# Performance work log

Measured on AMD Instinct MI355X. Metric: run time of the kernel, lower is better.

The kernel has to match this reference:

```python
import jax, jax.numpy as jnp
import numpy as np

F_DIM = 512   # feature_dim
H = 8         # num_heads
D = F_DIM // H  # attention_dim = 64
N = 12288     # total nodes
NP = 6144     # protein nodes (static)
NL = 3072     # ligand nodes (static)
EPS = 1e-5    # LayerNorm eps (torch default)


def setup_inputs() -> dict:
    key = jax.random.key(0)
    ks = jax.random.split(key, 12)
    g = lambda k, shape, s: (jax.random.normal(k, shape, jnp.float32) * s)
    return {
        "h": jax.random.normal(ks[0], (N, F_DIM), jnp.float32),
        # first NP active rows are protein (mask_ligand==0), next NL are ligand, rest inactive
        "mask_ligand": (jnp.arange(N) >= NP).astype(jnp.int32),
        "batch_mask": jnp.arange(N) < (NP + NL),
        "Wp": g(ks[1], (H, F_DIM, D), 0.04),   # per-head protein_linears (no bias)
        "Wl": g(ks[2], (H, F_DIM, D), 0.04),   # per-head ligand_linears (no bias)
        "Up_w": g(ks[3], (H, D, F_DIM), 0.1), "Up_b": g(ks[4], (H, F_DIM), 0.02),
        "Ul_w": g(ks[5], (H, D, F_DIM), 0.1), "Ul_b": g(ks[6], (H, F_DIM), 0.02),
        "ln_w": jnp.ones((D,), jnp.float32), "ln_b": jnp.zeros((D,), jnp.float32),
        "pg_w": g(ks[7], (F_DIM, D), 0.04), "pg_b": jnp.zeros((D,), jnp.float32),
        "lg_w": g(ks[8], (F_DIM, D), 0.04), "lg_b": jnp.zeros((D,), jnp.float32),
        "fb_w": g(ks[9], (D, D), 0.1), "fb_b": jnp.zeros((D,), jnp.float32),
        "fl_w": g(ks[10], (H * F_DIM, F_DIM), 0.015), "fl_b": g(ks[11], (F_DIM,), 0.02),
    }


def _layernorm(x, w, b):
    mu = x.mean(-1, keepdims=True)
    var = ((x - mu) ** 2).mean(-1, keepdims=True)
    return (x - mu) / jnp.sqrt(var + EPS) * w + b


def reference(h, mask_ligand, batch_mask, Wp, Wl, Up_w, Up_b, Ul_w, Ul_b,
              ln_w, ln_b, pg_w, pg_b, lg_w, lg_b, fb_w, fb_b, fl_w, fl_b):
    prot_idx = jnp.nonzero((mask_ligand == 0) & batch_mask, size=NP)[0]
    lig_idx = jnp.nonzero((mask_ligand == 1) & batch_mask, size=NL)[0]
    hp = h[prot_idx]   # [NP, F]
    hl = h[lig_idx]    # [NL, F]

    pf = jnp.einsum('nf,hfd->hnd', hp, Wp)              # per-head protein feats
    lf = jnp.einsum('mf,hfd->hmd', hl, Wl)              # per-head ligand feats
    scores = jnp.einsum('hnd,hmd->hnm', pf, lf) / (D ** 0.5)
    pa = jax.nn.softmax(scores, axis=-1)                # protein attends over ligand
    la = jax.nn.softmax(scores, axis=1)                 # ligand attends over protein
    pc = jnp.einsum('hnm,hmd->hnd', pa, lf)             # protein context
    lc = jnp.einsum('hnm,hnd->hmd', la, pf)             # ligand context

    # gates are head-independent in the original (recomputed identically per head)
    pgate = jax.nn.sigmoid(hp @ pg_w + pg_b)            # [NP, D]
    lgate = jax.nn.sigmoid(hl @ lg_w + lg_b)            # [NL, D]

    pc = jax.nn.sigmoid(_layernorm(pc * pgate, ln_w, ln_b) @ fb_w + fb_b)
    lc = jax.nn.sigmoid(_layernorm(lc * lgate, ln_w, ln_b) @ fb_w + fb_b)

    pout = jnp.einsum('hnd,hdf->hnf', pc, Up_w) + Up_b[:, None, :]
    lout = jnp.einsum('hmd,hdf->hmf', lc, Ul_w) + Ul_b[:, None, :]

    # concat per-head outputs along feature dim, then final projection
    p_final = pout.transpose(1, 0, 2).reshape(NP, H * F_DIM) @ fl_w + fl_b
    l_final = lout.transpose(1, 0, 2).reshape(NL, H * F_DIM) @ fl_w + fl_b

    h_updated = h.at[prot_idx].set(p_final + hp)
    h_updated = h_updated.at[lig_idx].set(l_final + hl)
    return h_updated
```

## Files before the change

kernel.cpp:

```cpp
#include <hip/hip_runtime.h>
#include <hip/hip_bf16.h>
#include <cstdint>
#include <cstddef>

#define F_DIM 512
#define NHEAD 8
#define DD 64
#define NPROT 6144
#define NLIG 3072
#define NACT 9216
#define NTOT 12288

typedef unsigned short u16;
typedef __attribute__((ext_vector_type(8))) short bf8;
typedef __attribute__((ext_vector_type(4))) float f4;

__device__ __forceinline__ u16 f2bf(float f){
  union { float f; uint32_t u; } v; v.f = f;
  uint32_t r = v.u + 0x7fffu + ((v.u >> 16) & 1u);
  return (u16)(r >> 16);
}

__device__ __forceinline__ f4 mfma16(bf8 a, bf8 b, f4 c){
  return __builtin_amdgcn_mfma_f32_16x16x32_bf16(a, b, c, 0, 0, 0);
}

__global__ void k_cvt(const float* __restrict__ in, u16* __restrict__ out, int n4){
  int i = blockIdx.x * blockDim.x + threadIdx.x;
  if (i >= n4) return;
  float4 v = ((const float4*)in)[i];
  union { u16 u[4]; uint64_t q; } pk;
  pk.u[0]=f2bf(v.x); pk.u[1]=f2bf(v.y); pk.u[2]=f2bf(v.z); pk.u[3]=f2bf(v.w);
  ((uint64_t*)out)[i] = pk.q;
}

__global__ __launch_bounds__(256) void k_cvtT64(const float* __restrict__ in,
                                                u16* __restrict__ out, int R, int C){
  __shared__ u16 T[64][65];
  int64_t base = (int64_t)blockIdx.z * R * C;
  int cb = blockIdx.x*64, rb = blockIdx.y*64;
  #pragma unroll
  for (int i=0;i<16;i++){
    int idx = i*256 + threadIdx.x;
    int r = idx>>6, c = idx&63;
    T[r][c] = f2bf(in[base + (int64_t)(rb+r)*C + cb + c]);
  }
  __syncthreads();
  #pragma unroll
  for (int i=0;i<16;i++){
    int idx = i*256 + threadIdx.x;
    int c = idx>>6, r = idx&63;
    out[base + (int64_t)(cb+c)*R + rb + r] = T[r][c];
  }
}

__global__ __launch_bounds__(256) void k_proj(const u16* __restrict__ hb,
    const u16* __restrict__ WpT, const u16* __restrict__ WlT,
    u16* __restrict__ pf, u16* __restrict__ pfT,
    u16* __restrict__ lfb, u16* __restrict__ lfT){
  int pass = blockIdx.z;
  if (pass == 1 && blockIdx.x >= NLIG/64) return;
  int M = pass ? NLIG : NPROT;
  const u16* A  = hb + (pass ? (size_t)NPROT*F_DIM : 0);
  const u16* BT = pass ? WlT : WpT;
  u16* P  = pass ? lfb : pf;
  u16* PT = pass ? lfT : pfT;
  int h = blockIdx.y;
  int w = threadIdx.x >> 6, lane = threadIdx.x & 63;
  int lr = lane & 15, lkg = lane >> 4, lk = lkg * 8;
  int rb = blockIdx.x * 64;
  const u16* Ap = A + (size_t)(rb + w*16 + lr) * F_DIM + lk;
  const u16* Bp = BT + (size_t)h * DD * F_DIM + (size_t)lr * F_DIM + lk;
  f4 acc[4] = {};
  for (int k = 0; k < F_DIM; k += 32){
    bf8 a = *(const bf8*)(Ap + k);
    #pragma unroll
    for (int cf = 0; cf < 4; cf++){
      bf8 b = *(const bf8*)(Bp + (size_t)cf*16*F_DIM + k);
      acc[cf] = mfma16(a, b, acc[cf]);
    }
  }
  __shared__ u16 T[64*72];
  #pragma unroll
  for (int cf = 0; cf < 4; cf++){
    int d = cf*16 + lr;
    #pragma unroll
    for (int r = 0; r < 4; r++){
      u16 v = f2bf(acc[cf][r]);
      int rl = w*16 + lkg*4 + r;
      P[(size_t)h*M*DD + (size_t)(rb+rl)*DD + d] = v;
      T[rl*72 + d] = v;
    }
  }
  __syncthreads();
  int d = threadIdx.x >> 2, j = threadIdx.x & 3;
  union { u16 u[16]; bf8 v[2]; } pk;
  #pragma unroll
  for (int uu = 0; uu < 16; uu++) pk.u[uu] = T[(j*16+uu)*72 + d];
  bf8* dst = (bf8*)(PT + ((size_t)h*DD + d)*M + rb + j*16);
  dst[0] = pk.v[0]; dst[1] = pk.v[1];
}

__global__ __launch_bounds__(256) void k_gate(const u16* __restrict__ hb,
    const u16* __restrict__ pgT, const u16* __restrict__ lgT,
    const float* __restrict__ pgb, const float* __restrict__ lgb,
    float* __restrict__ pgate, float* __restrict__ lgate){
  int pass = blockIdx.z;
  if (pass == 1 && blockIdx.x >= NLIG/64) return;
  const u16* A  = hb + (pass ? (size_t)NPROT*F_DIM : 0);
  const u16* BT = pass ? lgT : pgT;
  const float* gb = pass ? lgb : pgb;
  float* outp = pass ? lgate : pgate;
  int w = threadIdx.x>>6, lane = threadIdx.x&63, lr = lane&15, lkg = lane>>4, lk = lkg*8;
  int rb = blockIdx.x*64;
  const u16* Ap = A + (size_t)(rb + w*16 + lr)*F_DIM + lk;
  const u16* Bp = BT + (size_t)lr*F_DIM + lk;
  f4 acc[4] = {};
  for (int k=0;k<F_DIM;k+=32){
    bf8 a = *(const bf8*)(Ap+k);
    #pragma unroll
    for (int cf=0;cf<4;cf++){
      bf8 b = *(const bf8*)(Bp + (size_t)cf*16*F_DIM + k);
      acc[cf]=mfma16(a,b,acc[cf]);
    }
  }
  int r0 = rb + w*16 + lkg*4;
  #pragma unroll
  for (int cf=0;cf<4;cf++){
    int d = cf*16+lr; float bb = gb[d];
    #pragma unroll
    for (int r=0;r<4;r++){
      float z = acc[cf][r] + bb;
      outp[(size_t)(r0+r)*DD + d] = 1.f/(1.f + __expf(-z));
    }
  }
}

__global__ __launch_bounds__(256) void k_mw(const u16* __restrict__ UpWb, const u16* __restrict__ UlWb,
    const u16* __restrict__ flT, u16* __restrict__ MpT, u16* __restrict__ MlT){
  const u16* A = blockIdx.z ? UlWb : UpWb;
  u16* O = blockIdx.z ? MlT : MpT;
  int h = blockIdx.y;
  int fobase = blockIdx.x * 64;
  int w = threadIdx.x>>6, lane = threadIdx.x&63, lr = lane&15, lkg = lane>>4, lk = lkg*8;
  const u16* Ap = A + (size_t)h*DD*F_DIM + (size_t)(w*16+lr)*F_DIM + lk;
  const u16* Bp = flT + (size_t)(fobase+lr)*(NHEAD*F_DIM) + (size_t)h*F_DIM + lk;
  f4 acc[4] = {};
  for (int k=0;k<F_DIM;k+=32){
    bf8 a = *(const bf8*)(Ap+k);
    #pragma unroll
    for (int cf=0;cf<4;cf++){
      bf8 b = *(const bf8*)(Bp + (size_t)cf*16*(NHEAD*F_DIM) + k);
      acc[cf]=mfma16(a,b,acc[cf]);
    }
  }
  int d0 = w*16 + lkg*4;
  #pragma unroll
  for (int cf=0;cf<4;cf++){
    int fo = fobase + cf*16 + lr;
    #pragma unroll
    for (int r=0;r<4;r++)
      O[(size_t)fo*F_DIM + h*DD + d0 + r] = f2bf(acc[cf][r]);
  }
}

__global__ void k_cinit(const float* __restrict__ flb, float* __restrict__ cp, float* __restrict__ cl){
  int i = blockIdx.x*blockDim.x + threadIdx.x;
  if (i < F_DIM){ cp[i] = flb[i]; cl[i] = flb[i]; }
}
__global__ void k_cacc(const float* __restrict__ flw, const float* __restrict__ Upb,
    const float* __restrict__ Ulb, float* __restrict__ cp, float* __restrict__ cl){
  const float* bias = blockIdx.z ? Ulb : Upb;
  float* o = blockIdx.z ? cl : cp;
  int fo = blockIdx.y*256 + threadIdx.x;
  int r0 = blockIdx.x*512;
  float acc = 0.f;
  for (int r = r0; r < r0+512; r++) acc += bias[r] * flw[(size_t)r*F_DIM + fo];
  atomicAdd(o + fo, acc);
}

__global__ __launch_bounds__(256) void k_attn(
    const u16* __restrict__ pf, const u16* __restrict__ lfb,
    const u16* __restrict__ pfT, const u16* __restrict__ lfT,
    float* __restrict__ pnum, float* __restrict__ pden,
    float* __restrict__ lnum, float* __restrict__ lden){
  int bid = blockIdx.x;
  int pass = (bid >= 768);
  int NQ, NK, qt, chunk, h;
  const u16 *Q, *Kt, *Vt; float *num, *den;
  if (!pass){
    qt = bid >> 4; int rem = bid & 15; chunk = rem >> 3; h = rem & 7;
    NQ = NPROT; NK = NLIG; Q = pf; Kt = lfb; Vt = lfT; num = pnum; den = pden;
  } else {
    int l = bid - 768; qt = l >> 5; int rem = l & 31; chunk = rem >> 3; h = rem & 7;
    NQ = NLIG; NK = NPROT; Q = lfb; Kt = pf; Vt = pfT; num = lnum; den = lden;
  }
  int qbase = qt*128;
  int mb0 = chunk*1536;

  __shared__ u16 Pl[128*72];
  int w = threadIdx.x>>6, lane = threadIdx.x&63;
  int lr = lane&15, lkg = lane>>4, lk = lkg*8;
  u16* Pw = Pl + (w*32)*72;
  const u16* Qh = Q + (size_t)h*NQ*DD;
  const u16* Kh = Kt + (size_t)h*NK*DD;
  const u16* Vh = Vt + (size_t)h*DD*NK;

  int rA = qbase + w*16 + lr, rB = rA + 64;
  bf8 a0 = *(const bf8*)(Qh + (size_t)rA*DD + lk);
  bf8 a1 = *(const bf8*)(Qh + (size_t)rA*DD + 32 + lk);
  bf8 a2 = *(const bf8*)(Qh + (size_t)rB*DD + lk);
  bf8 a3 = *(const bf8*)(Qh + (size_t)rB*DD + 32 + lk);

  f4 accA[4] = {}, accB[4] = {};
  float raA[4] = {0,0,0,0}, raB[4] = {0,0,0,0};
  const float SC = 0.125f * 1.44269504088896f;

  for (int mb = mb0; mb < mb0 + 1536; mb += 64){
    f4 sA[4], sB[4];
    #pragma unroll
    for (int cf=0;cf<4;cf++){
      const u16* kp = Kh + (size_t)(mb + cf*16 + lr)*DD + lk;
      bf8 b0 = *(const bf8*)(kp);
      bf8 b1 = *(const bf8*)(kp + 32);
      f4 z = {}; z = mfma16(a0, b0, z); sA[cf] = mfma16(a1, b1, z);
      f4 y = {}; y = mfma16(a2, b0, y); sB[cf] = mfma16(a3, b1, y);
    }
    #pragma unroll
    for (int cf=0;cf<4;cf++){
      #pragma unroll
      for (int r=0;r<4;r++){
        float eA = exp2f(sA[cf][r]*SC); raA[r] += eA;
        Pw[(lkg*4+r)*72 + cf*16 + lr] = f2bf(eA);
        float eB = exp2f(sB[cf][r]*SC); raB[r] += eB;
        Pw[(16 + lkg*4+r)*72 + cf*16 + lr] = f2bf(eB);
      }
    }
    #pragma unroll
    for (int kc=0;kc<2;kc++){
      bf8 pA = *(const bf8*)(Pw + lr*72 + kc*32 + lk);
      bf8 pB = *(const bf8*)(Pw + (16+lr)*72 + kc*32 + lk);
      #pragma unroll
      for (int cf=0;cf<4;cf++){
        bf8 vb = *(const bf8*)(Vh + (size_t)(cf*16+lr)*NK + mb + kc*32 + lk);
        accA[cf] = mfma16(pA, vb, accA[cf]);
        accB[cf] = mfma16(pB, vb, accB[cf]);
      }
    }
  }

  #pragma unroll
  for (int r=0;r<4;r++){
    float t = raA[r];
    t += __shfl_xor(t,1,64); t += __shfl_xor(t,2,64);
    t += __shfl_xor(t,4,64); t += __shfl_xor(t,8,64);
    raA[r] = t;
    float u = raB[r];
    u += __shfl_xor(u,1,64); u += __shfl_xor(u,2,64);
    u += __shfl_xor(u,4,64); u += __shfl_xor(u,8,64);
    raB[r] = u;
  }
  int oA = qbase + w*16 + lkg*4, oB = oA + 64;
  if (lr == 0){
    #pragma unroll
    for (int r=0;r<4;r++){
      atomicAdd(&den[(size_t)h*NQ + oA + r], raA[r]);
      atomicAdd(&den[(size_t)h*NQ + oB + r], raB[r]);
    }
  }
  #pragma unroll
  for (int cf=0;cf<4;cf++){
    int d = cf*16 + lr;
    #pragma unroll
    for (int r=0;r<4;r++){
      atomicAdd(&num[((size_t)h*NQ + oA + r)*DD + d], accA[cf][r]);
      atomicAdd(&num[((size_t)h*NQ + oB + r)*DD + d], accB[cf][r]);
    }
  }
}

__global__ __launch_bounds__(256) void k_post(
    const float* __restrict__ pnum, const float* __restrict__ pden,
    const float* __restrict__ lnum, const float* __restrict__ lden,
    const float* __restrict__ pgate, const float* __restrict__ lgate,
    const float* __restrict__ lnw, const float* __restrict__ lnb,
    const u16* __restrict__ fbT, const float* __restrict__ fbb,
    u16* __restrict__ pc2, u16* __restrict__ lc2){
  int t = blockIdx.x;
  int pass = (t >= NPROT/64);
  int h = blockIdx.y;
  int NQ = pass ? NLIG : NPROT;
  const float* num = pass ? lnum : pnum;
  const float* den = pass ? lden : pden;
  const float* gate = pass ? lgate : pgate;
  u16* oc = pass ? lc2 : pc2;
  int qbase = (pass ? t - NPROT/64 : t) * 64;

  __shared__ u16 Pl[64*72];
  int w = threadIdx.x>>6, lane = threadIdx.x&63;
  int lr = lane&15, lkg = lane>>4, lk = lkg*8;
  u16* Pw = Pl + (w*16)*72;
  int orow0 = qbase + w*16 + lkg*4;

  float rd[4];
  #pragma unroll
  for (int r=0;r<4;r++) rd[r] = 1.f / den[(size_t)h*NQ + orow0 + r];

  float v[4][4];
  #pragma unroll
  for (int cf=0;cf<4;cf++){
    int d = cf*16+lr;
    #pragma unroll
    for (int r=0;r<4;r++)
      v[cf][r] = num[((size_t)h*NQ + orow0 + r)*DD + d] * rd[r]
               * gate[(size_t)(orow0+r)*DD + d];
  }
  float m1[4], m2[4];
  #pragma unroll
  for (int r=0;r<4;r++){
    float s1 = v[0][r]+v[1][r]+v[2][r]+v[3][r];
    float s2 = v[0][r]*v[0][r]+v[1][r]*v[1][r]+v[2][r]*v[2][r]+v[3][r]*v[3][r];
    s1 += __shfl_xor(s1,1,64); s2 += __shfl_xor(s2,1,64);
    s1 += __shfl_xor(s1,2,64); s2 += __shfl_xor(s2,2,64);
    s1 += __shfl_xor(s1,4,64); s2 += __shfl_xor(s2,4,64);
    s1 += __shfl_xor(s1,8,64); s2 += __shfl_xor(s2,8,64);
    float mu = s1 * (1.f/64.f);
    float var = s2 * (1.f/64.f) - mu*mu;
    if (var < 0.f) var = 0.f;
    m1[r] = mu; m2[r] = rsqrtf(var + 1e-5f);
  }
  #pragma unroll
  for (int cf=0;cf<4;cf++){
    int d = cf*16+lr;
    float lw = lnw[d], lb = lnb[d];
    #pragma unroll
    for (int r=0;r<4;r++){
      float n = (v[cf][r]-m1[r])*m2[r]*lw + lb;
      Pw[(lkg*4+r)*72 + d] = f2bf(n);
    }
  }
  f4 z4[4] = {};
  #pragma unroll
  for (int kc=0;kc<2;kc++){
    bf8 pa = *(const bf8*)(Pw + lr*72 + kc*32 + lk);
    #pragma unroll
    for (int cf=0;cf<4;cf++){
      bf8 b = *(const bf8*)(fbT + (size_t)(cf*16+lr)*DD + kc*32 + lk);
      z4[cf] = mfma16(pa, b, z4[cf]);
    }
  }
  #pragma unroll
  for (int cf=0;cf<4;cf++){
    int d = cf*16+lr;
    float bb = fbb[d];
    #pragma unroll
    for (int r=0;r<4;r++){
      float sg = 1.f/(1.f + __expf(-(z4[cf][r] + bb)));
      oc[(size_t)(orow0+r)*F_DIM + h*DD + d] = f2bf(sg);
    }
  }
}

__global__ __launch_bounds__(256) void k_final(const float* __restrict__ hsrc,
    const u16* __restrict__ pc2, const u16* __restrict__ lc2,
    const u16* __restrict__ MpT, const u16* __restrict__ MlT,
    const float* __restrict__ cp, const float* __restrict__ cl,
    float* __restrict__ out){
  int R = blockIdx.x*64;
  int cbase = blockIdx.y*64;
  int tid = threadIdx.x;
  if (R >= NACT){
    int r = tid>>2, s0 = tid&3;
    const float4* hp4 = (const float4*)(hsrc + (size_t)(R+r)*F_DIM + cbase);
    float4* op4 = (float4*)(out + (size_t)(R+r)*F_DIM + cbase);
    #pragma unroll
    for (int s=0;s<4;s++) op4[s0 + s*4] = hp4[s0 + s*4];
    return;
  }
  bool isP = (R < NPROT);
  const u16* A = isP ? (pc2 + (size_t)R*F_DIM) : (lc2 + (size_t)(R-NPROT)*F_DIM);
  const u16* B = isP ? MpT : MlT;
  const float* cv = isP ? cp : cl;
  int w = tid>>6, lane = tid&63, lr = lane&15, lkg = lane>>4, lk = lkg*8;
  const u16* Ap = A + (size_t)(w*16+lr)*F_DIM + lk;
  const u16* Bp = B + (size_t)(cbase+lr)*F_DIM + lk;
  f4 acc[4] = {};
  for (int k=0;k<F_DIM;k+=32){
    bf8 a = *(const bf8*)(Ap+k);
    #pragma unroll
    for (int cf=0;cf<4;cf++){
      bf8 b = *(const bf8*)(Bp + (size_t)cf*16*F_DIM + k);
      acc[cf]=mfma16(a,b,acc[cf]);
    }
  }
  int row0 = R + w*16 + lkg*4;
  #pragma unroll
  for (int cf=0;cf<4;cf++){
    int c = cbase + cf*16 + lr;
    float cc = cv[c];
    #pragma unroll
    for (int r=0;r<4;r++)
      out[(size_t)(row0+r)*F_DIM + c] = acc[cf][r] + cc + hsrc[(size_t)(row0+r)*F_DIM + c];
  }
}

extern "C" void kernel_launch(void* const* d_in, const int* in_sizes, int n_in,
                              void* d_out, int out_size, void* d_ws, size_t ws_size,
                              hipStream_t stream){
  (void)in_sizes; (void)n_in; (void)out_size; (void)ws_size;
  const float* h    = (const float*)d_in[0];
  const float* Wp   = (const float*)d_in[3];
  const float* Wl   = (const float*)d_in[4];
  const float* Upw  = (const float*)d_in[5];
  const float* Upb  = (const float*)d_in[6];
  const float* Ulw  = (const float*)d_in[7];
  const float* Ulb  = (const float*)d_in[8];
  const float* lnw  = (const float*)d_in[9];
  const float* lnb  = (const float*)d_in[10];
  const float* pgw  = (const float*)d_in[11];
  const float* pgb  = (const float*)d_in[12];
  const float* lgw  = (const float*)d_in[13];
  const float* lgb  = (const float*)d_in[14];
  const float* fbw  = (const float*)d_in[15];
  const float* fbb  = (const float*)d_in[16];
  const float* flw  = (const float*)d_in[17];
  const float* flb  = (const float*)d_in[18];
  float* out = (float*)d_out;

  char* wsp = (char*)d_ws;
  size_t off = 0;
  auto alloc = [&](size_t b)->char* {
    char* p = wsp + off; off = (off + b + 255) & ~(size_t)255; return p;
  };
  u16* hb    = (u16*)alloc((size_t)NACT*F_DIM*2);
  u16* WpT   = (u16*)alloc((size_t)NHEAD*DD*F_DIM*2);
  u16* WlT   = (u16*)alloc((size_t)NHEAD*DD*F_DIM*2);
  u16* pgT   = (u16*)alloc((size_t)DD*F_DIM*2);
  u16* lgT   = (u16*)alloc((size_t)DD*F_DIM*2);
  u16* fbT   = (u16*)alloc((size_t)DD*DD*2);
  u16* UpWb  = (u16*)alloc((size_t)NHEAD*DD*F_DIM*2);
  u16* UlWb  = (u16*)alloc((size_t)NHEAD*DD*F_DIM*2);
  u16* flT   = (u16*)alloc((size_t)F_DIM*NHEAD*F_DIM*2);
  u16* pf    = (u16*)alloc((size_t)NHEAD*NPROT*DD*2);
  u16* pfT   = (u16*)alloc((size_t)NHEAD*DD*NPROT*2);
  u16* lfb   = (u16*)alloc((size_t)NHEAD*NLIG*DD*2);
  u16* lfT   = (u16*)alloc((size_t)NHEAD*DD*NLIG*2);
  float* pgate = (float*)alloc((size_t)NPROT*DD*4);
  float* lgate = (float*)alloc((size_t)NLIG*DD*4);
  u16* pc2   = (u16*)alloc((size_t)NPROT*F_DIM*2);
  u16* lc2   = (u16*)alloc((size_t)NLIG*F_DIM*2);
  u16* MpT   = (u16*)alloc((size_t)F_DIM*F_DIM*2);
  u16* MlT   = (u16*)alloc((size_t)F_DIM*F_DIM*2);
  float* cp  = (float*)alloc(F_DIM*4);
  float* cl  = (float*)alloc(F_DIM*4);
  size_t n_pnum = (size_t)NHEAD*NPROT*DD, n_lnum = (size_t)NHEAD*NLIG*DD;
  size_t n_pden = (size_t)NHEAD*NPROT,     n_lden = (size_t)NHEAD*NLIG;
  size_t accN = n_pnum + n_lnum + n_pden + n_lden;
  float* accbuf = (float*)alloc(accN*4);
  float* pnum = accbuf;
  float* lnum = pnum + n_pnum;
  float* pden = lnum + n_lnum;
  float* lden = pden + n_pden;

  hipMemsetAsync(accbuf, 0, accN*4, stream);

  k_cvt<<<dim3((NACT*F_DIM/4 + 255)/256), 256, 0, stream>>>(h, hb, NACT*F_DIM/4);
  k_cvt<<<dim3((NHEAD*DD*F_DIM/4 + 255)/256), 256, 0, stream>>>(Upw, UpWb, NHEAD*DD*F_DIM/4);
  k_cvt<<<dim3((NHEAD*DD*F_DIM/4 + 255)/256), 256, 0, stream>>>(Ulw, UlWb, NHEAD*DD*F_DIM/4);
  k_cvtT64<<<dim3(1, 8, NHEAD), 256, 0, stream>>>(Wp, WpT, F_DIM, DD);
  k_cvtT64<<<dim3(1, 8, NHEAD), 256, 0, stream>>>(Wl, WlT, F_DIM, DD);
  k_cvtT64<<<dim3(1, 8, 1), 256, 0, stream>>>(pgw, pgT, F_DIM, DD);
  k_cvtT64<<<dim3(1, 8, 1), 256, 0, stream>>>(lgw, lgT, F_DIM, DD);
  k_cvtT64<<<dim3(1, 1, 1), 256, 0, stream>>>(fbw, fbT, DD, DD);
  k_cvtT64<<<dim3(8, 64, 1), 256, 0, stream>>>(flw, flT, NHEAD*F_DIM, F_DIM);

  k_proj<<<dim3(NPROT/64, NHEAD, 2), 256, 0, stream>>>(hb, WpT, WlT, pf, pfT, lfb, lfT);
  k_gate<<<dim3(NPROT/64, 1, 2), 256, 0, stream>>>(hb, pgT, lgT, pgb, lgb, pgate, lgate);
  k_mw<<<dim3(F_DIM/64, NHEAD, 2), 256, 0, stream>>>(UpWb, UlWb, flT, MpT, MlT);
  k_cinit<<<dim3(2), 256, 0, stream>>>(flb, cp, cl);
  k_cacc<<<dim3(8, 2, 2), 256, 0, stream>>>(flw, Upb, Ulb, cp, cl);

  k_attn<<<dim3(1536), 256, 0, stream>>>(pf, lfb, pfT, lfT, pnum, pden, lnum, lden);
  k_post<<<dim3(NPROT/64 + NLIG/64, NHEAD), 256, 0, stream>>>(
      pnum, pden, lnum, lden, pgate, lgate, lnw, lnb, fbT, fbb, pc2, lc2);
  k_final<<<dim3(NTOT/64, F_DIM/64), 256, 0, stream>>>(h, pc2, lc2, MpT, MlT, cp, cl, out);
}
```

Baseline: 574.1 us.

## Rewrite attention kernel with 32x32 MFMA and register-only P via permlane swap

The attention kernel moves from 16x16x32 MFMA with an LDS round-trip for the exponentiated scores to 32x32x16 MFMA computing S^T directly. P is repacked into B-operand layout in registers using v_cvt_pk_bf16 and permlane32_swap, which removes shared memory and its barriers-free stores and loads. It also uses raw v_exp_f32 and adds launch bounds with occupancy 2. The k_cacc bias-fold kernel is split into more blocks with smaller row ranges, and the inline asm exp relies on a fixed s_nop for hazard avoidance.

```diff
diff --git a/kernel.cpp b/kernel.cpp
--- a/kernel.cpp
+++ b/kernel.cpp
@@ -14,6 +14,8 @@
 typedef unsigned short u16;
 typedef __attribute__((ext_vector_type(8))) short bf8;
 typedef __attribute__((ext_vector_type(4))) float f4;
+typedef __attribute__((ext_vector_type(16))) float f16f;
+typedef __attribute__((ext_vector_type(2))) unsigned int u32x2;
 
 __device__ __forceinline__ u16 f2bf(float f){
   union { float f; uint32_t u; } v; v.f = f;
@@ -23,6 +25,17 @@
 
 __device__ __forceinline__ f4 mfma16(bf8 a, bf8 b, f4 c){
   return __builtin_amdgcn_mfma_f32_16x16x32_bf16(a, b, c, 0, 0, 0);
+}
+
+__device__ __forceinline__ float exp2_fast(float x){
+  float r;
+  asm volatile("v_exp_f32 %0, %1\n\ts_nop 1" : "=v"(r) : "v"(x));
+  return r;
+}
+__device__ __forceinline__ uint32_t cvtpk(float a, float b){
+  uint32_t r;
+  asm("v_cvt_pk_bf16_f32 %0, %1, %2" : "=v"(r) : "v"(a), "v"(b));
+  return r;
 }
 
 __global__ void k_cvt(const float* __restrict__ in, u16* __restrict__ out, int n4){
@@ -173,13 +186,14 @@
   const float* bias = blockIdx.z ? Ulb : Upb;
   float* o = blockIdx.z ? cl : cp;
   int fo = blockIdx.y*256 + threadIdx.x;
-  int r0 = blockIdx.x*512;
+  int r0 = blockIdx.x*128;
   float acc = 0.f;
-  for (int r = r0; r < r0+512; r++) acc += bias[r] * flw[(size_t)r*F_DIM + fo];
+  #pragma unroll 4
+  for (int r = r0; r < r0+128; r++) acc += bias[r] * flw[(size_t)r*F_DIM + fo];
   atomicAdd(o + fo, acc);
 }
 
-__global__ __launch_bounds__(256) void k_attn(
+__global__ __launch_bounds__(256, 2) void k_attn(
     const u16* __restrict__ pf, const u16* __restrict__ lfb,
     const u16* __restrict__ pfT, const u16* __restrict__ lfT,
     float* __restrict__ pnum, float* __restrict__ pden,
@@ -195,87 +209,66 @@
     int l = bid - 768; qt = l >> 5; int rem = l & 31; chunk = rem >> 3; h = rem & 7;
     NQ = NLIG; NK = NPROT; Q = lfb; Kt = pf; Vt = pfT; num = lnum; den = lden;
   }
-  int qbase = qt*128;
-  int mb0 = chunk*1536;
-
-  __shared__ u16 Pl[128*72];
-  int w = threadIdx.x>>6, lane = threadIdx.x&63;
-  int lr = lane&15, lkg = lane>>4, lk = lkg*8;
-  u16* Pw = Pl + (w*32)*72;
+  int wv = threadIdx.x>>6, lane = threadIdx.x&63;
+  int ql = lane&31, hi = lane>>5;
+  int qg = qt*128 + wv*32 + ql;
   const u16* Qh = Q + (size_t)h*NQ*DD;
   const u16* Kh = Kt + (size_t)h*NK*DD;
   const u16* Vh = Vt + (size_t)h*DD*NK;
-
-  int rA = qbase + w*16 + lr, rB = rA + 64;
-  bf8 a0 = *(const bf8*)(Qh + (size_t)rA*DD + lk);
-  bf8 a1 = *(const bf8*)(Qh + (size_t)rA*DD + 32 + lk);
-  bf8 a2 = *(const bf8*)(Qh + (size_t)rB*DD + lk);
-  bf8 a3 = *(const bf8*)(Qh + (size_t)rB*DD + 32 + lk);
-
-  f4 accA[4] = {}, accB[4] = {};
-  float raA[4] = {0,0,0,0}, raB[4] = {0,0,0,0};
   const float SC = 0.125f * 1.44269504088896f;
 
-  for (int mb = mb0; mb < mb0 + 1536; mb += 64){
-    f4 sA[4], sB[4];
-    #pragma unroll
-    for (int cf=0;cf<4;cf++){
-      const u16* kp = Kh + (size_t)(mb + cf*16 + lr)*DD + lk;
-      bf8 b0 = *(const bf8*)(kp);
-      bf8 b1 = *(const bf8*)(kp + 32);
-      f4 z = {}; z = mfma16(a0, b0, z); sA[cf] = mfma16(a1, b1, z);
-      f4 y = {}; y = mfma16(a2, b0, y); sB[cf] = mfma16(a3, b1, y);
-    }
-    #pragma unroll
-    for (int cf=0;cf<4;cf++){
-      #pragma unroll
-      for (int r=0;r<4;r++){
-        float eA = exp2f(sA[cf][r]*SC); raA[r] += eA;
-        Pw[(lkg*4+r)*72 + cf*16 + lr] = f2bf(eA);
-        float eB = exp2f(sB[cf][r]*SC); raB[r] += eB;
-        Pw[(16 + lkg*4+r)*72 + cf*16 + lr] = f2bf(eB);
-      }
-    }
-    #pragma unroll
-    for (int kc=0;kc<2;kc++){
-      bf8 pA = *(const bf8*)(Pw + lr*72 + kc*32 + lk);
-      bf8 pB = *(const bf8*)(Pw + (16+lr)*72 + kc*32 + lk);
-      #pragma unroll
-      for (int cf=0;cf<4;cf++){
-        bf8 vb = *(const bf8*)(Vh + (size_t)(cf*16+lr)*NK + mb + kc*32 + lk);
-        accA[cf] = mfma16(pA, vb, accA[cf]);
-        accB[cf] = mfma16(pB, vb, accB[cf]);
-      }
-    }
-  }
-
-  #pragma unroll
-  for (int r=0;r<4;r++){
-    float t = raA[r];
-    t += __shfl_xor(t,1,64); t += __shfl_xor(t,2,64);
-    t += __shfl_xor(t,4,64); t += __shfl_xor(t,8,64);
-    raA[r] = t;
-    float u = raB[r];
-    u += __shfl_xor(u,1,64); u += __shfl_xor(u,2,64);
-    u += __shfl_xor(u,4,64); u += __shfl_xor(u,8,64);
-    raB[r] = u;
-  }
-  int oA = qbase + w*16 + lkg*4, oB = oA + 64;
-  if (lr == 0){
-    #pragma unroll
-    for (int r=0;r<4;r++){
-      atomicAdd(&den[(size_t)h*NQ + oA + r], raA[r]);
-      atomicAdd(&den[(size_t)h*NQ + oB + r], raB[r]);
-    }
-  }
-  #pragma unroll
-  for (int cf=0;cf<4;cf++){
-    int d = cf*16 + lr;
-    #pragma unroll
-    for (int r=0;r<4;r++){
-      atomicAdd(&num[((size_t)h*NQ + oA + r)*DD + d], accA[cf][r]);
-      atomicAdd(&num[((size_t)h*NQ + oB + r)*DD + d], accB[cf][r]);
-    }
+  bf8 qf[4];
+  #pragma unroll
+  for (int kk=0;kk<4;kk++)
+    qf[kk] = *(const bf8*)(Qh + (size_t)qg*DD + kk*16 + hi*8);
+
+  f16f o0 = {}, o1 = {};
+  float dsum = 0.f;
+  int kv0 = chunk*1536;
+  const u16* Kp  = Kh + (size_t)(kv0 + ql)*DD + hi*8;
+  const u16* Vp0 = Vh + (size_t)ql*NK + kv0 + hi*8;
+  const u16* Vp1 = Vh + (size_t)(32+ql)*NK + kv0 + hi*8;
+
+  for (int t=0; t<48; t++){
+    f16f s = {};
+    #pragma unroll
+    for (int kk=0;kk<4;kk++){
+      bf8 kf = *(const bf8*)(Kp + kk*16);
+      s = __builtin_amdgcn_mfma_f32_32x32x16_bf16(kf, qf[kk], s, 0, 0, 0);
+    }
+    float e[16];
+    #pragma unroll
+    for (int r=0;r<16;r++){ e[r] = exp2_fast(s[r]*SC); dsum += e[r]; }
+    union { uint32_t u[4]; bf8 v; } B0, B1;
+    {
+      u32x2 p;
+      p = __builtin_amdgcn_permlane32_swap(cvtpk(e[0],e[1]),   cvtpk(e[4],e[5]),   false, false);
+      B0.u[0]=p[0]; B0.u[2]=p[1];
+      p = __builtin_amdgcn_permlane32_swap(cvtpk(e[2],e[3]),   cvtpk(e[6],e[7]),   false, false);
+      B0.u[1]=p[0]; B0.u[3]=p[1];
+      p = __builtin_amdgcn_permlane32_swap(cvtpk(e[8],e[9]),   cvtpk(e[12],e[13]), false, false);
+      B1.u[0]=p[0]; B1.u[2]=p[1];
+      p = __builtin_amdgcn_permlane32_swap(cvtpk(e[10],e[11]), cvtpk(e[14],e[15]), false, false);
+      B1.u[1]=p[0]; B1.u[3]=p[1];
+    }
+    bf8 v00 = *(const bf8*)(Vp0);
+    bf8 v01 = *(const bf8*)(Vp0 + 16);
+    bf8 v10 = *(const bf8*)(Vp1);
+    bf8 v11 = *(const bf8*)(Vp1 + 16);
+    o0 = __builtin_amdgcn_mfma_f32_32x32x16_bf16(v00, B0.v, o0, 0, 0, 0);
+    o0 = __builtin_amdgcn_mfma_f32_32x32x16_bf16(v01, B1.v, o0, 0, 0, 0);
+    o1 = __builtin_amdgcn_mfma_f32_32x32x16_bf16(v10, B0.v, o1, 0, 0, 0);
+    o1 = __builtin_amdgcn_mfma_f32_32x32x16_bf16(v11, B1.v, o1, 0, 0, 0);
+    Kp += 32*DD; Vp0 += 32; Vp1 += 32;
+  }
+
+  atomicAdd(&den[(size_t)h*NQ + qg], dsum);
+  float* np = num + ((size_t)h*NQ + qg)*DD;
+  #pragma unroll
+  for (int r=0;r<16;r++){
+    int d = (r&3) + 8*(r>>2) + 4*hi;
+    atomicAdd(np + d,      o0[r]);
+    atomicAdd(np + 32 + d, o1[r]);
   }
 }
 
@@ -478,7 +471,7 @@
   k_gate<<<dim3(NPROT/64, 1, 2), 256, 0, stream>>>(hb, pgT, lgT, pgb, lgb, pgate, lgate);
   k_mw<<<dim3(F_DIM/64, NHEAD, 2), 256, 0, stream>>>(UpWb, UlWb, flT, MpT, MlT);
   k_cinit<<<dim3(2), 256, 0, stream>>>(flb, cp, cl);
-  k_cacc<<<dim3(8, 2, 2), 256, 0, stream>>>(flw, Upb, Ulb, cp, cl);
+  k_cacc<<<dim3(32, 2, 2), 256, 0, stream>>>(flw, Upb, Ulb, cp, cl);
 
   k_attn<<<dim3(1536), 256, 0, stream>>>(pf, lfb, pfT, lfT, pnum, pden, lnum, lden);
   k_post<<<dim3(NPROT/64 + NLIG/64, NHEAD), 256, 0, stream>>>(
```

Measured after the change: 804.7 us. 40.2% more time.
